# Kernel optimization log

Hardware: AMD Instinct MI355X
Metric: run time of the kernel (lower is better)

The kernel has to match this reference:

```python
import jax, jax.numpy as jnp
import numpy as np

N = 262144   # number of feature vectors to tokenize
Q = 8        # n_quantizers
K = 1024     # codebook_size
D = 64       # feature_size


def setup_inputs() -> dict:
    key = jax.random.key(0)
    k1, k2 = jax.random.split(key)
    x = jax.random.normal(k1, (N, D), dtype=jnp.float32)
    # matches torch init: (rand - 0.5) * 2  in [-1, 1]
    codebooks = (jax.random.uniform(k2, (Q, K, D), dtype=jnp.float32) - 0.5) * 2.0
    return {"x": x, "codebooks": codebooks}


def reference(x, codebooks):
    """RVQTokenizer.encode: residual VQ over Q stages.

    Returns (encoded [N, Q] int32, quantized [N, D] float32).
    argmin over squared distances == argmin over cdist (monotone), so we use
    the expansion ||r||^2 - 2 r.c + ||c||^2 and never take a sqrt.
    """
    n_q = codebooks.shape[0]
    quantized = jnp.zeros_like(x)
    codes = []
    for j in range(n_q):  # small fixed loop over quantizer stages
        r = x - quantized                                  # [N, D] residual
        cb = codebooks[j]                                  # [K, D]
        # squared euclidean distances, [N, K]
        d2 = (jnp.sum(r * r, axis=-1, keepdims=True)
              - 2.0 * (r @ cb.T)
              + jnp.sum(cb * cb, axis=-1))
        idx = jnp.argmin(d2, axis=1)                       # [N]
        codes.append(idx)
        quantized = quantized + cb[idx]                    # gather-accumulate
    encoded = jnp.stack(codes, axis=1)                     # [N, Q]
    return encoded, quantized
```

## Files before the change

kernel.cpp:

```cpp
#include <hip/hip_runtime.h>
#include <float.h>
#include <stdint.h>

#define QN 8
#define KN 1024
#define DN 64
#define MARGIN 1.5e-3f

typedef float    f32x16 __attribute__((ext_vector_type(16)));
typedef _Float16 f16x8  __attribute__((ext_vector_type(8)));

union AB8 { uint4 v; uint32_t u[4]; f16x8 h; };

__device__ __forceinline__ float np_sumsq64(const float* a) {
    float p[DN];
    #pragma unroll
    for (int t = 0; t < DN; ++t) p[t] = __fmul_rn(a[t], a[t]);
    float l1[32];
    #pragma unroll
    for (int t = 0; t < 32; ++t) l1[t] = __fadd_rn(p[t], p[t + 32]);
    float l2[16];
    #pragma unroll
    for (int t = 0; t < 16; ++t) l2[t] = __fadd_rn(l1[t], l1[t + 16]);
    float l3[8];
    #pragma unroll
    for (int t = 0; t < 8; ++t) l3[t] = __fadd_rn(l2[t], l2[t + 8]);
    float l4[4];
    #pragma unroll
    for (int t = 0; t < 4; ++t) l4[t] = __fadd_rn(l3[t], l3[t + 4]);
    const float l5a = __fadd_rn(l4[0], l4[2]);
    const float l5b = __fadd_rn(l4[1], l4[3]);
    return __fadd_rn(l5a, l5b);
}

__device__ __forceinline__ float rr_tree(const float rex[DN]) {
    float l1[32];
    #pragma unroll
    for (int t = 0; t < 32; ++t)
        l1[t] = __fadd_rn(__fmul_rn(rex[t], rex[t]), __fmul_rn(rex[t+32], rex[t+32]));
    float l2[16];
    #pragma unroll
    for (int t = 0; t < 16; ++t) l2[t] = __fadd_rn(l1[t], l1[t + 16]);
    float l3[8];
    #pragma unroll
    for (int t = 0; t < 8; ++t) l3[t] = __fadd_rn(l2[t], l2[t + 8]);
    float l4[4];
    #pragma unroll
    for (int t = 0; t < 4; ++t) l4[t] = __fadd_rn(l3[t], l3[t + 4]);
    return __fadd_rn(__fadd_rn(l4[0], l4[2]), __fadd_rn(l4[1], l4[3]));
}

__device__ __attribute__((noinline)) int full_exact_call(
    int j, const float* __restrict__ xrow, const float* __restrict__ cb,
    const float* __restrict__ cnj,
    int c0, int c1, int c2, int c3, int c4, int c5, int c6, int c7) {
    int cs[QN] = {c0, c1, c2, c3, c4, c5, c6, c7};
    float rex[DN];
    #pragma unroll
    for (int d4 = 0; d4 < DN / 4; ++d4) {
        const float4 xv = *(const float4*)(xrow + 4 * d4);
        float q0 = 0.f, q1 = 0.f, q2 = 0.f, q3 = 0.f;
        #pragma unroll
        for (int l = 0; l < QN; ++l) {
            const float4 cv = *(const float4*)(
                cb + ((size_t)l * KN + cs[l]) * DN + 4 * d4);
            const bool p = (l < j);
            q0 = p ? __fadd_rn(q0, cv.x) : q0;
            q1 = p ? __fadd_rn(q1, cv.y) : q1;
            q2 = p ? __fadd_rn(q2, cv.z) : q2;
            q3 = p ? __fadd_rn(q3, cv.w) : q3;
        }
        rex[4*d4+0] = __fsub_rn(xv.x, q0); rex[4*d4+1] = __fsub_rn(xv.y, q1);
        rex[4*d4+2] = __fsub_rn(xv.z, q2); rex[4*d4+3] = __fsub_rn(xv.w, q3);
    }
    const float rr = rr_tree(rex);

    const float* cbj = cb + (size_t)j * KN * DN;
    float bd = FLT_MAX; int bk = 0;
    #pragma unroll 1
    for (int k = 0; k < KN; k += 4) {
        float cr0 = 0.f, cr1 = 0.f, cr2 = 0.f, cr3 = 0.f;
        const float* p0 = cbj + (size_t)(k + 0) * DN;
        const float* p1 = cbj + (size_t)(k + 1) * DN;
        const float* p2 = cbj + (size_t)(k + 2) * DN;
        const float* p3 = cbj + (size_t)(k + 3) * DN;
        #pragma unroll
        for (int d4 = 0; d4 < DN / 4; ++d4) {
            const float4 a = *(const float4*)(p0 + 4 * d4);
            const float4 b = *(const float4*)(p1 + 4 * d4);
            const float4 c = *(const float4*)(p2 + 4 * d4);
            const float4 e = *(const float4*)(p3 + 4 * d4);
            const float r0 = rex[4*d4+0], r1 = rex[4*d4+1];
            const float r2 = rex[4*d4+2], r3 = rex[4*d4+3];
            cr0 = __fmaf_rn(r0, a.x, cr0); cr0 = __fmaf_rn(r1, a.y, cr0);
            cr0 = __fmaf_rn(r2, a.z, cr0); cr0 = __fmaf_rn(r3, a.w, cr0);
            cr1 = __fmaf_rn(r0, b.x, cr1); cr1 = __fmaf_rn(r1, b.y, cr1);
            cr1 = __fmaf_rn(r2, b.z, cr1); cr1 = __fmaf_rn(r3, b.w, cr1);
            cr2 = __fmaf_rn(r0, c.x, cr2); cr2 = __fmaf_rn(r1, c.y, cr2);
            cr2 = __fmaf_rn(r2, c.z, cr2); cr2 = __fmaf_rn(r3, c.w, cr2);
            cr3 = __fmaf_rn(r0, e.x, cr3); cr3 = __fmaf_rn(r1, e.y, cr3);
            cr3 = __fmaf_rn(r2, e.z, cr3); cr3 = __fmaf_rn(r3, e.w, cr3);
        }
        const float d20 = __fadd_rn(__fsub_rn(rr, __fmul_rn(2.0f, cr0)), cnj[k + 0]);
        const float d21 = __fadd_rn(__fsub_rn(rr, __fmul_rn(2.0f, cr1)), cnj[k + 1]);
        const float d22 = __fadd_rn(__fsub_rn(rr, __fmul_rn(2.0f, cr2)), cnj[k + 2]);
        const float d23 = __fadd_rn(__fsub_rn(rr, __fmul_rn(2.0f, cr3)), cnj[k + 3]);
        if (d20 < bd) { bd = d20; bk = k + 0; }
        if (d21 < bd) { bd = d21; bk = k + 1; }
        if (d22 < bd) { bd = d22; bk = k + 2; }
        if (d23 < bd) { bd = d23; bk = k + 3; }
    }
    return bk;
}

__global__ __launch_bounds__(256) void rvq_prep_kernel(const float* __restrict__ cb,
                                                       uint32_t* __restrict__ apackH,
                                                       uint32_t* __restrict__ apackL,
                                                       float* __restrict__ cn) {
    const int cidx = (int)blockIdx.x * 256 + (int)threadIdx.x;
    if (cidx >= QN * KN) return;
    float row[DN];
    const float4* cp = (const float4*)(cb + (size_t)cidx * DN);
    #pragma unroll
    for (int d4 = 0; d4 < DN / 4; ++d4) {
        const float4 v = cp[d4];
        row[4*d4+0] = v.x; row[4*d4+1] = v.y; row[4*d4+2] = v.z; row[4*d4+3] = v.w;
    }
    cn[cidx] = np_sumsq64(row);

    const int j = cidx >> 10, local = cidx & 1023;
    const int c = local >> 5, col = local & 31;
    #pragma unroll
    for (int kk = 0; kk < 4; ++kk) {
        #pragma unroll
        for (int hh = 0; hh < 2; ++hh) {
            AB8 uh, ul;
            #pragma unroll
            for (int e = 0; e < 8; ++e) {
                const float v = -2.0f * row[kk * 16 + hh * 8 + e];
                const _Float16 hi = (_Float16)v;
                const float hr = (float)hi;
                const _Float16 lo = (_Float16)__fsub_rn(v, hr);
                uh.h[e] = hi; ul.h[e] = lo;
            }
            const size_t off = (((size_t)(j * 32 + c) * 4 + kk) * 256
                                + (((hh << 5) | col) << 2));
            *(uint4*)(apackH + off) = uh.v;
            *(uint4*)(apackL + off) = ul.v;
        }
    }
}

#define INSV(sv, ixv, B1v, I1v, B2v, I2v, B3v) do {                          \
    const bool lt1 = (sv) < B1v, lt2 = (sv) < B2v;                           \
    B3v = __builtin_amdgcn_fmed3f((sv), B2v, B3v);                           \
    B2v = __builtin_amdgcn_fmed3f((sv), B1v, B2v);                           \
    I2v = lt1 ? I1v : (lt2 ? (ixv) : I2v);                                   \
    B1v = fminf((sv), B1v);                                                  \
    I1v = lt1 ? (ixv) : I1v;                                                 \
} while (0)

__device__ __forceinline__ void splitpack2(float a, float b, uint32_t& H, uint32_t& L) {
    const _Float16 ah = (_Float16)a; const float ar = (float)ah;
    const _Float16 al = (_Float16)__fsub_rn(a, ar);
    const _Float16 bh = (_Float16)b; const float br = (float)bh;
    const _Float16 bl = (_Float16)__fsub_rn(b, br);
    H = (uint32_t)__builtin_bit_cast(uint16_t, ah)
      | ((uint32_t)__builtin_bit_cast(uint16_t, bh) << 16);
    L = (uint32_t)__builtin_bit_cast(uint16_t, al)
      | ((uint32_t)__builtin_bit_cast(uint16_t, bl) << 16);
}

__global__ __launch_bounds__(256, 3) void rvq_encode_kernel(
    const float* __restrict__ x, const float* __restrict__ cb,
    const uint32_t* __restrict__ apackH, const uint32_t* __restrict__ apackL,
    const float* __restrict__ cnref,
    float* __restrict__ out_enc, float* __restrict__ out_q, int n) {
    const int tid  = (int)threadIdx.x;
    const int lane = tid & 63;
    const int wid  = tid >> 6;
    const int h    = lane >> 5;
    const int iv   = (int)blockIdx.x * 128 + wid * 32 + (lane & 31);
    const int ivs  = iv < n ? iv : (n - 1);
    const float* xrow = x + (size_t)ivs * DN;

    float x_[32], q_[32];
    #pragma unroll
    for (int kk = 0; kk < 4; ++kk) {
        const float4 a = *(const float4*)(xrow + kk * 16 + 8 * h);
        const float4 b = *(const float4*)(xrow + kk * 16 + 8 * h + 4);
        x_[kk*8+0] = a.x; x_[kk*8+1] = a.y; x_[kk*8+2] = a.z; x_[kk*8+3] = a.w;
        x_[kk*8+4] = b.x; x_[kk*8+5] = b.y; x_[kk*8+6] = b.z; x_[kk*8+7] = b.w;
    }
    #pragma unroll
    for (int t = 0; t < 32; ++t) q_[t] = 0.f;

    int codes[QN] = {0, 0, 0, 0, 0, 0, 0, 0};

    #pragma unroll
    for (int j = 0; j < QN; ++j) {
        uint32_t bhU[16], blU[16];
        {
            float rloc[32];
            #pragma unroll
            for (int t = 0; t < 32; ++t) rloc[t] = __fsub_rn(x_[t], q_[t]);
            #pragma unroll
            for (int kk = 0; kk < 4; ++kk)
                #pragma unroll
                for (int m = 0; m < 4; ++m)
                    splitpack2(rloc[kk*8+2*m], rloc[kk*8+2*m+1],
                               bhU[kk*4+m], blU[kk*4+m]);
        }

        float b1 = FLT_MAX, b2 = FLT_MAX, b3 = FLT_MAX; int i1 = 0, i2 = 0;

        const uint32_t* aH  = apackH + (size_t)j * 32768;
        const uint32_t* aL  = apackL + (size_t)j * 32768;
        const float*    cnj = cnref + (size_t)j * KN;

        #pragma unroll 1
        for (int ch = 0; ch < 32; ++ch) {
            f32x16 acc;
            #pragma unroll
            for (int q = 0; q < 4; ++q) {
                const float4 t = *(const float4*)(cnj + ch * 32 + q * 8 + h * 4);
                acc[4*q+0] = t.x; acc[4*q+1] = t.y; acc[4*q+2] = t.z; acc[4*q+3] = t.w;
            }
            #pragma unroll
            for (int kk = 0; kk < 4; ++kk) {
                AB8 ah_, al_, bh_, bl_;
                ah_.v = *(const uint4*)(aH + (size_t)(ch * 4 + kk) * 256 + lane * 4);
                al_.v = *(const uint4*)(aL + (size_t)(ch * 4 + kk) * 256 + lane * 4);
                bh_.u[0] = bhU[kk*4+0]; bh_.u[1] = bhU[kk*4+1];
                bh_.u[2] = bhU[kk*4+2]; bh_.u[3] = bhU[kk*4+3];
                bl_.u[0] = blU[kk*4+0]; bl_.u[1] = blU[kk*4+1];
                bl_.u[2] = blU[kk*4+2]; bl_.u[3] = blU[kk*4+3];
                acc = __builtin_amdgcn_mfma_f32_32x32x16_f16(ah_.h, bh_.h, acc, 0, 0, 0);
                acc = __builtin_amdgcn_mfma_f32_32x32x16_f16(al_.h, bh_.h, acc, 0, 0, 0);
                acc = __builtin_amdgcn_mfma_f32_32x32x16_f16(ah_.h, bl_.h, acc, 0, 0, 0);
            }
            const int ibase = ch * 32 + 4 * h;
            #pragma unroll
            for (int q = 0; q < 16; ++q) {
                const int ix = ibase + (q & 3) + 8 * (q >> 2);
                const float s = acc[q];
                INSV(s, ix, b1, i1, b2, i2, b3);
            }
        }

        {
            const float pb1 = __shfl_xor(b1, 32, 64); const int pi1 = __shfl_xor(i1, 32, 64);
            const float pb2 = __shfl_xor(b2, 32, 64); const int pi2 = __shfl_xor(i2, 32, 64);
            const float pb3 = __shfl_xor(b3, 32, 64);
            INSV(pb1, pi1, b1, i1, b2, i2, b3);
            INSV(pb2, pi2, b1, i1, b2, i2, b3);
            INSV(pb3, 0,   b1, i1, b2, i2, b3);
        }

        int chosen = i1;
        if (__builtin_expect(b2 - b1 < MARGIN, 0)) {
            if (__builtin_expect(b3 - b1 < MARGIN, 0)) {
                chosen = full_exact_call(j, xrow, cb, cnj,
                                         codes[0], codes[1], codes[2], codes[3],
                                         codes[4], codes[5], codes[6], codes[7]);
            } else {
                float rloc[32], po[32];
                #pragma unroll
                for (int t = 0; t < 32; ++t) rloc[t] = __fsub_rn(x_[t], q_[t]);
                #pragma unroll
                for (int t = 0; t < 32; ++t) po[t] = __shfl_xor(rloc[t], 32, 64);
                float rex[DN];
                #pragma unroll
                for (int kk = 0; kk < 4; ++kk)
                    #pragma unroll
                    for (int e = 0; e < 8; ++e) {
                        rex[kk*16 + e]     = h ? po[kk*8+e]   : rloc[kk*8+e];
                        rex[kk*16 + 8 + e] = h ? rloc[kk*8+e] : po[kk*8+e];
                    }
                const float rr = rr_tree(rex);

                const float* cbj = cb + (size_t)j * KN * DN;
                const float* c0p = cbj + (size_t)i1 * DN;
                const float* c1p = cbj + (size_t)i2 * DN;
                float cr0 = 0.f, cr1 = 0.f;
                #pragma unroll
                for (int d4 = 0; d4 < DN / 4; ++d4) {
                    const float4 a = *(const float4*)(c0p + 4 * d4);
                    const float4 b = *(const float4*)(c1p + 4 * d4);
                    cr0 = __fmaf_rn(rex[4*d4+0], a.x, cr0); cr1 = __fmaf_rn(rex[4*d4+0], b.x, cr1);
                    cr0 = __fmaf_rn(rex[4*d4+1], a.y, cr0); cr1 = __fmaf_rn(rex[4*d4+1], b.y, cr1);
                    cr0 = __fmaf_rn(rex[4*d4+2], a.z, cr0); cr1 = __fmaf_rn(rex[4*d4+2], b.z, cr1);
                    cr0 = __fmaf_rn(rex[4*d4+3], a.w, cr0); cr1 = __fmaf_rn(rex[4*d4+3], b.w, cr1);
                }
                const float d2c0 = __fadd_rn(__fsub_rn(rr, __fmul_rn(2.0f, cr0)), cnj[i1]);
                const float d2c1 = __fadd_rn(__fsub_rn(rr, __fmul_rn(2.0f, cr1)), cnj[i2]);
                float bd = d2c0; int bk = i1;
                if (d2c1 < bd || (d2c1 == bd && i2 < bk)) { bd = d2c1; bk = i2; }
                chosen = bk;
            }
        }
        codes[j] = chosen;

        {
            const float* cw = cb + ((size_t)j * KN + chosen) * DN;
            #pragma unroll
            for (int kk = 0; kk < 4; ++kk) {
                const float4 a = *(const float4*)(cw + kk * 16 + 8 * h);
                const float4 b = *(const float4*)(cw + kk * 16 + 8 * h + 4);
                q_[kk*8+0] = __fadd_rn(q_[kk*8+0], a.x);
                q_[kk*8+1] = __fadd_rn(q_[kk*8+1], a.y);
                q_[kk*8+2] = __fadd_rn(q_[kk*8+2], a.z);
                q_[kk*8+3] = __fadd_rn(q_[kk*8+3], a.w);
                q_[kk*8+4] = __fadd_rn(q_[kk*8+4], b.x);
                q_[kk*8+5] = __fadd_rn(q_[kk*8+5], b.y);
                q_[kk*8+6] = __fadd_rn(q_[kk*8+6], b.z);
                q_[kk*8+7] = __fadd_rn(q_[kk*8+7], b.w);
            }
        }
    }

    if (iv < n) {
        if (h == 0) {
            float4 e0, e1;
            e0.x = (float)codes[0]; e0.y = (float)codes[1];
            e0.z = (float)codes[2]; e0.w = (float)codes[3];
            e1.x = (float)codes[4]; e1.y = (float)codes[5];
            e1.z = (float)codes[6]; e1.w = (float)codes[7];
            *(float4*)(out_enc + (size_t)iv * QN)     = e0;
            *(float4*)(out_enc + (size_t)iv * QN + 4) = e1;
        }
        float4* qo = (float4*)(out_q + (size_t)iv * DN);
        #pragma unroll
        for (int kk = 0; kk < 4; ++kk) {
            float4 o0, o1;
            o0.x = q_[kk*8+0]; o0.y = q_[kk*8+1]; o0.z = q_[kk*8+2]; o0.w = q_[kk*8+3];
            o1.x = q_[kk*8+4]; o1.y = q_[kk*8+5]; o1.z = q_[kk*8+6]; o1.w = q_[kk*8+7];
            qo[kk*4 + 2*h]     = o0;
            qo[kk*4 + 2*h + 1] = o1;
        }
    }
}

extern "C" void kernel_launch(void* const* d_in, const int* in_sizes, int n_in,
                              void* d_out, int out_size, void* d_ws, size_t ws_size,
                              hipStream_t stream) {
    const float* x   = (const float*)d_in[0];
    const float* cbp = (const float*)d_in[1];
    const int n = in_sizes[0] / DN;

    float* out_enc = (float*)d_out;
    float* out_q   = (float*)d_out + (size_t)n * QN;

    uint32_t* apackH = (uint32_t*)d_ws;
    uint32_t* apackL = (uint32_t*)((char*)d_ws + (size_t)QN * KN * DN * 2);
    float*    cn     = (float*)((char*)d_ws + (size_t)QN * KN * DN * 4);

    rvq_prep_kernel<<<dim3((QN * KN + 255) / 256), dim3(256), 0, stream>>>(
        cbp, apackH, apackL, cn);
    rvq_encode_kernel<<<dim3((n + 127) / 128), dim3(256), 0, stream>>>(
        x, cbp, apackH, apackL, cn, out_enc, out_q, n);
}
```

Baseline: 1.329 ms.

## Pack indices into score low bits and parallelize exact fallback across wave

Packs each candidate's local index into the low mantissa bits of its MFMA score, so the top-4 selection is done with med3/min on floats alone and no per-candidate index selects are needed. Widens the tie margin and verifies the top three candidates exactly. In the rare deep-tie case it replaces the per-lane serial full 1024-entry scan with a wave-cooperative scan of 16 entries per lane followed by a shuffle reduction. The j loop is no longer unrolled to reduce code size and register pressure. Truncating score mantissas adds quantization noise, which the larger margin and B1CAP guard are meant to absorb, at the cost of more frequent fallback checks.

```diff
diff --git a/kernel.cpp b/kernel.cpp
--- a/kernel.cpp
+++ b/kernel.cpp
@@ -5,7 +5,9 @@
 #define QN 8
 #define KN 1024
 #define DN 64
-#define MARGIN 1.5e-3f
+#define MARGIN  1.0e-2f
+#define B1CAP   119.0f
+#define KEYMASK 0xFFFFFE00u
 
 typedef float    f32x16 __attribute__((ext_vector_type(16)));
 typedef _Float16 f16x8  __attribute__((ext_vector_type(8)));
@@ -48,69 +50,6 @@
     #pragma unroll
     for (int t = 0; t < 4; ++t) l4[t] = __fadd_rn(l3[t], l3[t + 4]);
     return __fadd_rn(__fadd_rn(l4[0], l4[2]), __fadd_rn(l4[1], l4[3]));
-}
-
-__device__ __attribute__((noinline)) int full_exact_call(
-    int j, const float* __restrict__ xrow, const float* __restrict__ cb,
-    const float* __restrict__ cnj,
-    int c0, int c1, int c2, int c3, int c4, int c5, int c6, int c7) {
-    int cs[QN] = {c0, c1, c2, c3, c4, c5, c6, c7};
-    float rex[DN];
-    #pragma unroll
-    for (int d4 = 0; d4 < DN / 4; ++d4) {
-        const float4 xv = *(const float4*)(xrow + 4 * d4);
-        float q0 = 0.f, q1 = 0.f, q2 = 0.f, q3 = 0.f;
-        #pragma unroll
-        for (int l = 0; l < QN; ++l) {
-            const float4 cv = *(const float4*)(
-                cb + ((size_t)l * KN + cs[l]) * DN + 4 * d4);
-            const bool p = (l < j);
-            q0 = p ? __fadd_rn(q0, cv.x) : q0;
-            q1 = p ? __fadd_rn(q1, cv.y) : q1;
-            q2 = p ? __fadd_rn(q2, cv.z) : q2;
-            q3 = p ? __fadd_rn(q3, cv.w) : q3;
-        }
-        rex[4*d4+0] = __fsub_rn(xv.x, q0); rex[4*d4+1] = __fsub_rn(xv.y, q1);
-        rex[4*d4+2] = __fsub_rn(xv.z, q2); rex[4*d4+3] = __fsub_rn(xv.w, q3);
-    }
-    const float rr = rr_tree(rex);
-
-    const float* cbj = cb + (size_t)j * KN * DN;
-    float bd = FLT_MAX; int bk = 0;
-    #pragma unroll 1
-    for (int k = 0; k < KN; k += 4) {
-        float cr0 = 0.f, cr1 = 0.f, cr2 = 0.f, cr3 = 0.f;
-        const float* p0 = cbj + (size_t)(k + 0) * DN;
-        const float* p1 = cbj + (size_t)(k + 1) * DN;
-        const float* p2 = cbj + (size_t)(k + 2) * DN;
-        const float* p3 = cbj + (size_t)(k + 3) * DN;
-        #pragma unroll
-        for (int d4 = 0; d4 < DN / 4; ++d4) {
-            const float4 a = *(const float4*)(p0 + 4 * d4);
-            const float4 b = *(const float4*)(p1 + 4 * d4);
-            const float4 c = *(const float4*)(p2 + 4 * d4);
-            const float4 e = *(const float4*)(p3 + 4 * d4);
-            const float r0 = rex[4*d4+0], r1 = rex[4*d4+1];
-            const float r2 = rex[4*d4+2], r3 = rex[4*d4+3];
-            cr0 = __fmaf_rn(r0, a.x, cr0); cr0 = __fmaf_rn(r1, a.y, cr0);
-            cr0 = __fmaf_rn(r2, a.z, cr0); cr0 = __fmaf_rn(r3, a.w, cr0);
-            cr1 = __fmaf_rn(r0, b.x, cr1); cr1 = __fmaf_rn(r1, b.y, cr1);
-            cr1 = __fmaf_rn(r2, b.z, cr1); cr1 = __fmaf_rn(r3, b.w, cr1);
-            cr2 = __fmaf_rn(r0, c.x, cr2); cr2 = __fmaf_rn(r1, c.y, cr2);
-            cr2 = __fmaf_rn(r2, c.z, cr2); cr2 = __fmaf_rn(r3, c.w, cr2);
-            cr3 = __fmaf_rn(r0, e.x, cr3); cr3 = __fmaf_rn(r1, e.y, cr3);
-            cr3 = __fmaf_rn(r2, e.z, cr3); cr3 = __fmaf_rn(r3, e.w, cr3);
-        }
-        const float d20 = __fadd_rn(__fsub_rn(rr, __fmul_rn(2.0f, cr0)), cnj[k + 0]);
-        const float d21 = __fadd_rn(__fsub_rn(rr, __fmul_rn(2.0f, cr1)), cnj[k + 1]);
-        const float d22 = __fadd_rn(__fsub_rn(rr, __fmul_rn(2.0f, cr2)), cnj[k + 2]);
-        const float d23 = __fadd_rn(__fsub_rn(rr, __fmul_rn(2.0f, cr3)), cnj[k + 3]);
-        if (d20 < bd) { bd = d20; bk = k + 0; }
-        if (d21 < bd) { bd = d21; bk = k + 1; }
-        if (d22 < bd) { bd = d22; bk = k + 2; }
-        if (d23 < bd) { bd = d23; bk = k + 3; }
-    }
-    return bk;
 }
 
 __global__ __launch_bounds__(256) void rvq_prep_kernel(const float* __restrict__ cb,
@@ -150,15 +89,6 @@
         }
     }
 }
-
-#define INSV(sv, ixv, B1v, I1v, B2v, I2v, B3v) do {                          \
-    const bool lt1 = (sv) < B1v, lt2 = (sv) < B2v;                           \
-    B3v = __builtin_amdgcn_fmed3f((sv), B2v, B3v);                           \
-    B2v = __builtin_amdgcn_fmed3f((sv), B1v, B2v);                           \
-    I2v = lt1 ? I1v : (lt2 ? (ixv) : I2v);                                   \
-    B1v = fminf((sv), B1v);                                                  \
-    I1v = lt1 ? (ixv) : I1v;                                                 \
-} while (0)
 
 __device__ __forceinline__ void splitpack2(float a, float b, uint32_t& H, uint32_t& L) {
     const _Float16 ah = (_Float16)a; const float ar = (float)ah;
@@ -170,6 +100,14 @@
     L = (uint32_t)__builtin_bit_cast(uint16_t, al)
       | ((uint32_t)__builtin_bit_cast(uint16_t, bl) << 16);
 }
+
+#define INS4IX(v, i) do {                                                    \
+    const bool lt1 = (v) < b1, lt2 = (v) < b2, lt3 = (v) < b3;               \
+    b4 = __builtin_amdgcn_fmed3f((v), b3, b4);                               \
+    b3 = __builtin_amdgcn_fmed3f((v), b2, b3); i3 = lt2 ? i2 : (lt3 ? (i) : i3); \
+    b2 = __builtin_amdgcn_fmed3f((v), b1, b2); i2 = lt1 ? i1 : (lt2 ? (i) : i2); \
+    b1 = fminf((v), b1);                       i1 = lt1 ? (i) : i1;          \
+} while (0)
 
 __global__ __launch_bounds__(256, 3) void rvq_encode_kernel(
     const float* __restrict__ x, const float* __restrict__ cb,
@@ -195,24 +133,21 @@
     #pragma unroll
     for (int t = 0; t < 32; ++t) q_[t] = 0.f;
 
-    int codes[QN] = {0, 0, 0, 0, 0, 0, 0, 0};
-
-    #pragma unroll
+    int codes[QN];
+
+    #pragma unroll 1
     for (int j = 0; j < QN; ++j) {
         uint32_t bhU[16], blU[16];
-        {
-            float rloc[32];
-            #pragma unroll
-            for (int t = 0; t < 32; ++t) rloc[t] = __fsub_rn(x_[t], q_[t]);
-            #pragma unroll
-            for (int kk = 0; kk < 4; ++kk)
-                #pragma unroll
-                for (int m = 0; m < 4; ++m)
-                    splitpack2(rloc[kk*8+2*m], rloc[kk*8+2*m+1],
-                               bhU[kk*4+m], blU[kk*4+m]);
-        }
-
-        float b1 = FLT_MAX, b2 = FLT_MAX, b3 = FLT_MAX; int i1 = 0, i2 = 0;
+        #pragma unroll
+        for (int kk = 0; kk < 4; ++kk)
+            #pragma unroll
+            for (int m = 0; m < 4; ++m) {
+                const float ra = __fsub_rn(x_[kk*8+2*m],   q_[kk*8+2*m]);
+                const float rb = __fsub_rn(x_[kk*8+2*m+1], q_[kk*8+2*m+1]);
+                splitpack2(ra, rb, bhU[kk*4+m], blU[kk*4+m]);
+            }
+
+        float k1 = FLT_MAX, k2 = FLT_MAX, k3 = FLT_MAX, k4 = FLT_MAX;
 
         const uint32_t* aH  = apackH + (size_t)j * 32768;
         const uint32_t* aL  = apackL + (size_t)j * 32768;
@@ -239,66 +174,140 @@
                 acc = __builtin_amdgcn_mfma_f32_32x32x16_f16(al_.h, bh_.h, acc, 0, 0, 0);
                 acc = __builtin_amdgcn_mfma_f32_32x32x16_f16(ah_.h, bl_.h, acc, 0, 0, 0);
             }
-            const int ibase = ch * 32 + 4 * h;
+            const uint32_t lb = (uint32_t)(ch * 16);
             #pragma unroll
             for (int q = 0; q < 16; ++q) {
-                const int ix = ibase + (q & 3) + 8 * (q >> 2);
-                const float s = acc[q];
-                INSV(s, ix, b1, i1, b2, i2, b3);
-            }
-        }
-
+                const uint32_t key = (__float_as_uint(acc[q]) & KEYMASK) | (lb + (uint32_t)q);
+                const float kf = __uint_as_float(key);
+                k4 = __builtin_amdgcn_fmed3f(kf, k3, k4);
+                k3 = __builtin_amdgcn_fmed3f(kf, k2, k3);
+                k2 = __builtin_amdgcn_fmed3f(kf, k1, k2);
+                k1 = fminf(kf, k1);
+            }
+        }
+
+        float b1 = k1, b2 = k2, b3 = k3, b4 = k4;
+        const int hb = 4 * h, hp = 4 * (1 - h);
+        int i1, i2, i3;
         {
-            const float pb1 = __shfl_xor(b1, 32, 64); const int pi1 = __shfl_xor(i1, 32, 64);
-            const float pb2 = __shfl_xor(b2, 32, 64); const int pi2 = __shfl_xor(i2, 32, 64);
-            const float pb3 = __shfl_xor(b3, 32, 64);
-            INSV(pb1, pi1, b1, i1, b2, i2, b3);
-            INSV(pb2, pi2, b1, i1, b2, i2, b3);
-            INSV(pb3, 0,   b1, i1, b2, i2, b3);
+            const uint32_t u1 = __float_as_uint(k1) & 511u;
+            const uint32_t u2 = __float_as_uint(k2) & 511u;
+            const uint32_t u3 = __float_as_uint(k3) & 511u;
+            i1 = (int)((u1 >> 4) * 32 + (u1 & 3) + 8 * ((u1 >> 2) & 3)) + hb;
+            i2 = (int)((u2 >> 4) * 32 + (u2 & 3) + 8 * ((u2 >> 2) & 3)) + hb;
+            i3 = (int)((u3 >> 4) * 32 + (u3 & 3) + 8 * ((u3 >> 2) & 3)) + hb;
+        }
+        {
+            const float p1 = __shfl_xor(k1, 32, 64);
+            const float p2 = __shfl_xor(k2, 32, 64);
+            const float p3 = __shfl_xor(k3, 32, 64);
+            const float p4 = __shfl_xor(k4, 32, 64);
+            const uint32_t v1 = __float_as_uint(p1) & 511u;
+            const uint32_t v2 = __float_as_uint(p2) & 511u;
+            const uint32_t v3 = __float_as_uint(p3) & 511u;
+            const int pi1 = (int)((v1 >> 4) * 32 + (v1 & 3) + 8 * ((v1 >> 2) & 3)) + hp;
+            const int pi2 = (int)((v2 >> 4) * 32 + (v2 & 3) + 8 * ((v2 >> 2) & 3)) + hp;
+            const int pi3 = (int)((v3 >> 4) * 32 + (v3 & 3) + 8 * ((v3 >> 2) & 3)) + hp;
+            INS4IX(p1, pi1);
+            INS4IX(p2, pi2);
+            INS4IX(p3, pi3);
+            INS4IX(p4, 0);
+        }
+        {
+            const int src = lane & 31;
+            b1 = __shfl(b1, src, 64); b2 = __shfl(b2, src, 64);
+            b3 = __shfl(b3, src, 64); b4 = __shfl(b4, src, 64);
+            i1 = __shfl(i1, src, 64); i2 = __shfl(i2, src, 64); i3 = __shfl(i3, src, 64);
         }
 
         int chosen = i1;
-        if (__builtin_expect(b2 - b1 < MARGIN, 0)) {
-            if (__builtin_expect(b3 - b1 < MARGIN, 0)) {
-                chosen = full_exact_call(j, xrow, cb, cnj,
-                                         codes[0], codes[1], codes[2], codes[3],
-                                         codes[4], codes[5], codes[6], codes[7]);
-            } else {
-                float rloc[32], po[32];
+        const bool near_ = (b2 - b1 < MARGIN);
+        const bool deep  = near_ && ((b4 - b1 < MARGIN) || (fabsf(b1) >= B1CAP));
+
+        if (__builtin_expect(near_ && !deep, 0)) {
+            float rl_[32], po[32];
+            #pragma unroll
+            for (int t = 0; t < 32; ++t) rl_[t] = __fsub_rn(x_[t], q_[t]);
+            #pragma unroll
+            for (int t = 0; t < 32; ++t) po[t] = __shfl_xor(rl_[t], 32, 64);
+            float rex[DN];
+            #pragma unroll
+            for (int kk = 0; kk < 4; ++kk)
                 #pragma unroll
-                for (int t = 0; t < 32; ++t) rloc[t] = __fsub_rn(x_[t], q_[t]);
+                for (int e = 0; e < 8; ++e) {
+                    rex[kk*16 + e]     = h ? po[kk*8+e]  : rl_[kk*8+e];
+                    rex[kk*16 + 8 + e] = h ? rl_[kk*8+e] : po[kk*8+e];
+                }
+            const float rr = rr_tree(rex);
+
+            const float* cbj = cb + (size_t)j * KN * DN;
+            const float* c0p = cbj + (size_t)i1 * DN;
+            const float* c1p = cbj + (size_t)i2 * DN;
+            const float* c2p = cbj + (size_t)i3 * DN;
+            float cr0 = 0.f, cr1 = 0.f, cr2 = 0.f;
+            #pragma unroll
+            for (int d4 = 0; d4 < DN / 4; ++d4) {
+                const float4 a = *(const float4*)(c0p + 4 * d4);
+                const float4 b = *(const float4*)(c1p + 4 * d4);
+                const float4 c = *(const float4*)(c2p + 4 * d4);
+                const float r0 = rex[4*d4+0], r1 = rex[4*d4+1];
+                const float r2 = rex[4*d4+2], r3 = rex[4*d4+3];
+                cr0 = __fmaf_rn(r0, a.x, cr0); cr1 = __fmaf_rn(r0, b.x, cr1); cr2 = __fmaf_rn(r0, c.x, cr2);
+                cr0 = __fmaf_rn(r1, a.y, cr0); cr1 = __fmaf_rn(r1, b.y, cr1); cr2 = __fmaf_rn(r1, c.y, cr2);
+                cr0 = __fmaf_rn(r2, a.z, cr0); cr1 = __fmaf_rn(r2, b.z, cr1); cr2 = __fmaf_rn(r2, c.z, cr2);
+                cr0 = __fmaf_rn(r3, a.w, cr0); cr1 = __fmaf_rn(r3, b.w, cr1); cr2 = __fmaf_rn(r3, c.w, cr2);
+            }
+            const float d2c0 = __fadd_rn(__fsub_rn(rr, __fmul_rn(2.0f, cr0)), cnj[i1]);
+            const float d2c1 = __fadd_rn(__fsub_rn(rr, __fmul_rn(2.0f, cr1)), cnj[i2]);
+            const float d2c2 = __fadd_rn(__fsub_rn(rr, __fmul_rn(2.0f, cr2)), cnj[i3]);
+            float bd = d2c0; int bk = i1;
+            if (d2c1 < bd || (d2c1 == bd && i2 < bk)) { bd = d2c1; bk = i2; }
+            if (d2c2 < bd || (d2c2 == bd && i3 < bk)) { bd = d2c2; bk = i3; }
+            chosen = bk;
+        }
+
+        unsigned long long dm = __ballot(deep) & 0xFFFFFFFFull;
+        while (__builtin_expect(dm != 0ull, 0)) {
+            const int p = __ffsll((long long)dm) - 1; dm &= dm - 1;
+            float rex[DN];
+            #pragma unroll
+            for (int kk = 0; kk < 4; ++kk)
                 #pragma unroll
-                for (int t = 0; t < 32; ++t) po[t] = __shfl_xor(rloc[t], 32, 64);
-                float rex[DN];
-                #pragma unroll
-                for (int kk = 0; kk < 4; ++kk)
-                    #pragma unroll
-                    for (int e = 0; e < 8; ++e) {
-                        rex[kk*16 + e]     = h ? po[kk*8+e]   : rloc[kk*8+e];
-                        rex[kk*16 + 8 + e] = h ? rloc[kk*8+e] : po[kk*8+e];
-                    }
-                const float rr = rr_tree(rex);
-
-                const float* cbj = cb + (size_t)j * KN * DN;
-                const float* c0p = cbj + (size_t)i1 * DN;
-                const float* c1p = cbj + (size_t)i2 * DN;
-                float cr0 = 0.f, cr1 = 0.f;
+                for (int e = 0; e < 8; ++e) {
+                    const float vloc = __fsub_rn(x_[kk*8+e], q_[kk*8+e]);
+                    rex[kk*16 + e]     = __shfl(vloc, p, 64);
+                    rex[kk*16 + 8 + e] = __shfl(vloc, p + 32, 64);
+                }
+            const float rr = rr_tree(rex);
+            const float* cbj = cb + (size_t)j * KN * DN;
+            const int k0 = lane * 16;
+            const float4* cn4 = (const float4*)(cnj + k0);
+            float bd = FLT_MAX; int bk = 0;
+            #pragma unroll 1
+            for (int t = 0; t < 16; ++t) {
+                const float* cp = cbj + (size_t)(k0 + t) * DN;
+                float cr = 0.f;
                 #pragma unroll
                 for (int d4 = 0; d4 < DN / 4; ++d4) {
-                    const float4 a = *(const float4*)(c0p + 4 * d4);
-                    const float4 b = *(const float4*)(c1p + 4 * d4);
-                    cr0 = __fmaf_rn(rex[4*d4+0], a.x, cr0); cr1 = __fmaf_rn(rex[4*d4+0], b.x, cr1);
-                    cr0 = __fmaf_rn(rex[4*d4+1], a.y, cr0); cr1 = __fmaf_rn(rex[4*d4+1], b.y, cr1);
-                    cr0 = __fmaf_rn(rex[4*d4+2], a.z, cr0); cr1 = __fmaf_rn(rex[4*d4+2], b.z, cr1);
-                    cr0 = __fmaf_rn(rex[4*d4+3], a.w, cr0); cr1 = __fmaf_rn(rex[4*d4+3], b.w, cr1);
+                    const float4 a = *(const float4*)(cp + 4 * d4);
+                    cr = __fmaf_rn(rex[4*d4+0], a.x, cr);
+                    cr = __fmaf_rn(rex[4*d4+1], a.y, cr);
+                    cr = __fmaf_rn(rex[4*d4+2], a.z, cr);
+                    cr = __fmaf_rn(rex[4*d4+3], a.w, cr);
                 }
-                const float d2c0 = __fadd_rn(__fsub_rn(rr, __fmul_rn(2.0f, cr0)), cnj[i1]);
-                const float d2c1 = __fadd_rn(__fsub_rn(rr, __fmul_rn(2.0f, cr1)), cnj[i2]);
-                float bd = d2c0; int bk = i1;
-                if (d2c1 < bd || (d2c1 == bd && i2 < bk)) { bd = d2c1; bk = i2; }
-                chosen = bk;
-            }
-        }
+                const float cnv = ((const float*)cn4)[t];
+                const float d2 = __fadd_rn(__fsub_rn(rr, __fmul_rn(2.0f, cr)), cnv);
+                if (d2 < bd) { bd = d2; bk = k0 + t; }
+            }
+            #pragma unroll
+            for (int off = 32; off; off >>= 1) {
+                const float od = __shfl_xor(bd, off, 64);
+                const int   ok = __shfl_xor(bk, off, 64);
+                if (od < bd || (od == bd && ok < bk)) { bd = od; bk = ok; }
+            }
+            if ((lane & 31) == p) chosen = bk;
+        }
+
         codes[j] = chosen;
 
         {
```

After: 1.514 ms. 14.0% more time.
